# Kernel optimization log

Measured on AMD Instinct MI355X. Metric: run time of the kernel, lower is better.

## Reference

```python
import jax, jax.numpy as jnp
import numpy as np

D = 1024
H = 16
HD = D // H
L = 2048
B = 1
MLP = 8192
ROPE_BASE = 10000.0
LN_EPS = 1e-5


def layer_norm(x):
    mu = jnp.mean(x, axis=-1, keepdims=True)
    var = jnp.var(x, axis=-1, keepdims=True)
    return (x - mu) / jnp.sqrt(var + LN_EPS)


def rope(x):
    # x: [B, H, L, HD]; non-traditional (rotate-half / NeoX style)
    half = HD // 2
    inv_freq = 1.0 / (ROPE_BASE ** (jnp.arange(0, half, dtype=jnp.float32) / half))
    pos = jnp.arange(x.shape[2], dtype=jnp.float32)
    ang = pos[:, None] * inv_freq[None, :]            # [L, half]
    cos, sin = jnp.cos(ang), jnp.sin(ang)
    x1, x2 = x[..., :half], x[..., half:]
    return jnp.concatenate([x1 * cos - x2 * sin, x2 * cos + x1 * sin], axis=-1).astype(x.dtype)


def setup_inputs() -> dict:
    key = jax.random.key(0)
    ks = jax.random.split(key, 5)
    x = jax.random.normal(ks[0], (B, L, D), dtype=jnp.float32)
    # causal additive mask
    neg = jnp.finfo(jnp.float32).min
    mask = jnp.where(jnp.tril(jnp.ones((L, L), dtype=bool)), 0.0, neg).astype(jnp.float32)
    W_attn = jax.random.normal(ks[1], (3 * D, D), dtype=jnp.float32) * (D ** -0.5)
    W_out = jax.random.normal(ks[2], (D, D), dtype=jnp.float32) * (D ** -0.5)
    W_ffp = jax.random.normal(ks[3], (MLP, D), dtype=jnp.float32) * (D ** -0.5)
    W_ffo = jax.random.normal(ks[4], (D, MLP // 2), dtype=jnp.float32) * ((MLP // 2) ** -0.5)
    return {"x": x, "mask": mask, "W_attn": W_attn, "W_out": W_out, "W_ffp": W_ffp, "W_ffo": W_ffo}


def block(x, mask, W_attn, W_out, W_ffp, W_ffo):
    b, l, d = x.shape
    scale = HD ** -0.5
    # attention branch
    xn = layer_norm(x)
    qkv = xn @ W_attn.T                                    # [B, L, 3D]
    q, k, v = jnp.split(qkv, 3, axis=-1)
    q = q.reshape(b, l, H, HD).transpose(0, 2, 1, 3)       # [B, H, L, HD]
    k = k.reshape(b, l, H, HD).transpose(0, 2, 1, 3)
    v = v.reshape(b, l, H, HD).transpose(0, 2, 1, 3)
    q = rope(q)
    k = rope(k)
    scores = jnp.einsum('bhqd,bhkd->bhqk', q * scale, k)   # [B, H, L, L]
    scores = scores + mask
    probs = jax.nn.softmax(scores.astype(jnp.float32), axis=-1).astype(scores.dtype)
    attn = jnp.einsum('bhqk,bhkd->bhqd', probs, v)
    attn = attn.transpose(0, 2, 1, 3).reshape(b, l, d)
    r = attn @ W_out.T
    h = x + r
    # SwiGLU MLP branch: split ff_proj output, swiglu(x2, x1) = silu(x2) * x1
    g = layer_norm(h) @ W_ffp.T                            # [B, L, MLP]
    x1, x2 = jnp.split(g, 2, axis=-1)
    mlp = (jax.nn.silu(x2) * x1) @ W_ffo.T
    return h + mlp


def reference(x, mask, W_attn, W_out, W_ffp, W_ffo):
    return block(x, mask, W_attn, W_out, W_ffp, W_ffo)
```

## Files before the change

kernel.cpp:

```cpp
#include <hip/hip_runtime.h>
#include <math.h>

#define DMODEL 1024
#define NHEAD  16
#define HDIM   64
#define SEQ    2048
#define MLPD   8192
#define HALF_MLP 4096
static constexpr float LN_EPS_C = 1e-5f;
#define NEG_BIG (-1e30f)
#define SM_SHIFT 16.0f

typedef short bf16x8 __attribute__((ext_vector_type(8)));
typedef float f32x4  __attribute__((ext_vector_type(4)));

__device__ __forceinline__ unsigned short f2b(float f) {
    unsigned int u = __float_as_uint(f);
    u = (u + 0x7FFFu + ((u >> 16) & 1u)) >> 16;
    return (unsigned short)u;
}
__device__ __forceinline__ float b2f(unsigned short h) {
    return __uint_as_float((unsigned int)h << 16);
}

__device__ __forceinline__ void async_copy16(const unsigned short* g, unsigned short* l) {
    __builtin_amdgcn_global_load_lds(
        (const __attribute__((address_space(1))) unsigned int*)(g),
        (__attribute__((address_space(3))) unsigned int*)(l),
        16, 0, 0);
}

__global__ void prep_all(const float* __restrict__ x,
                         const float* __restrict__ W_attn, const float* __restrict__ W_out,
                         const float* __restrict__ W_ffp,  const float* __restrict__ W_ffo,
                         unsigned short* __restrict__ xnb, float2* __restrict__ ct,
                         unsigned short* __restrict__ oa, unsigned short* __restrict__ ob,
                         unsigned short* __restrict__ oc, unsigned short* __restrict__ od) {
    const int bid = blockIdx.x;
    const int tid = threadIdx.x;
    if (bid < SEQ) {
        __shared__ float rs[256], rs2[256];
        float4 v = *(const float4*)(x + (size_t)bid * DMODEL + tid * 4);
        rs[tid]  = v.x + v.y + v.z + v.w;
        rs2[tid] = v.x * v.x + v.y * v.y + v.z * v.z + v.w * v.w;
        __syncthreads();
        for (int off = 128; off > 0; off >>= 1) {
            if (tid < off) { rs[tid] += rs[tid + off]; rs2[tid] += rs2[tid + off]; }
            __syncthreads();
        }
        float mu  = rs[0] * (1.0f / DMODEL);
        float var = rs2[0] * (1.0f / DMODEL) - mu * mu;
        float inv = rsqrtf(var + LN_EPS_C);
        ushort4 o;
        o.x = f2b((v.x - mu) * inv); o.y = f2b((v.y - mu) * inv);
        o.z = f2b((v.z - mu) * inv); o.w = f2b((v.w - mu) * inv);
        *(ushort4*)(xnb + (size_t)bid * DMODEL + tid * 4) = o;
    } else if (bid < SEQ + 256) {
        int idx = (bid - SEQ) * 256 + tid;
        int pos = idx >> 5, p = idx & 31;
        float invf = powf(10000.0f, -(float)p / 32.0f);
        float ang = (float)pos * invf;
        ct[idx] = make_float2(cosf(ang), sinf(ang));
    } else {
        const int n1 = 3 * DMODEL * DMODEL;
        const int n2 = n1 + DMODEL * DMODEL;
        const int n3 = n2 + MLPD * DMODEL;
        int i = ((bid - SEQ - 256) * 256 + tid) * 4;
        const float* src; unsigned short* dst; int off;
        if (i < n1)      { src = W_attn; dst = oa; off = i; }
        else if (i < n2) { src = W_out;  dst = ob; off = i - n1; }
        else if (i < n3) {
            src = W_ffp; off = i - n2;
            int row = off >> 10, col = off & 1023;
            int rp  = (row < HALF_MLP) ? (2 * row) : (2 * (row - HALF_MLP) + 1);
            float4 v = *(const float4*)(src + off);
            ushort4 o;
            o.x = f2b(v.x); o.y = f2b(v.y); o.z = f2b(v.z); o.w = f2b(v.w);
            *(ushort4*)(oc + ((size_t)rp << 10) + col) = o;
            return;
        }
        else             { src = W_ffo; dst = od; off = i - n3; }
        float4 v = *(const float4*)(src + off);
        ushort4 o;
        o.x = f2b(v.x); o.y = f2b(v.y); o.z = f2b(v.z); o.w = f2b(v.w);
        *(ushort4*)(dst + off) = o;
    }
}

__global__ void ln_red2(const float* __restrict__ p0, const float* __restrict__ p1,
                        const float* __restrict__ x, float* __restrict__ h,
                        unsigned short* __restrict__ xnb) {
    const int row = blockIdx.x;
    const int tid = threadIdx.x;
    __shared__ float rs[256], rs2[256];
    const size_t base = (size_t)row * DMODEL + tid * 4;
    float4 a = *(const float4*)(p0 + base);
    float4 b = *(const float4*)(p1 + base);
    float4 r = *(const float4*)(x + base);
    float4 v = { a.x + b.x + r.x, a.y + b.y + r.y, a.z + b.z + r.z, a.w + b.w + r.w };
    *(float4*)(h + base) = v;
    rs[tid]  = v.x + v.y + v.z + v.w;
    rs2[tid] = v.x * v.x + v.y * v.y + v.z * v.z + v.w * v.w;
    __syncthreads();
    for (int off = 128; off > 0; off >>= 1) {
        if (tid < off) { rs[tid] += rs[tid + off]; rs2[tid] += rs2[tid + off]; }
        __syncthreads();
    }
    float mu  = rs[0] * (1.0f / DMODEL);
    float var = rs2[0] * (1.0f / DMODEL) - mu * mu;
    float inv = rsqrtf(var + LN_EPS_C);
    ushort4 o;
    o.x = f2b((v.x - mu) * inv); o.y = f2b((v.y - mu) * inv);
    o.z = f2b((v.z - mu) * inv); o.w = f2b((v.w - mu) * inv);
    *(ushort4*)(xnb + base) = o;
}

__global__ __launch_bounds__(256)
void gemm_qkv(const unsigned short* __restrict__ A, const unsigned short* __restrict__ B,
              const float2* __restrict__ ct,
              unsigned short* __restrict__ Qp, unsigned short* __restrict__ Kp,
              unsigned short* __restrict__ Vt) {
    __shared__ unsigned short As[128 * 32];
    __shared__ unsigned short Bs[128 * 32];
    __shared__ unsigned short St[4][16][72];
    const int tid  = threadIdx.x;
    const int lane = tid & 63;
    const int w    = tid >> 6;
    const int wm   = w >> 1;
    const int wn   = w & 1;
    const int m0   = blockIdx.y * 128;
    const int n0   = blockIdx.x * 128;

    f32x4 acc[4][4] = {};

    const int srow = lane >> 2;
    const int scol = (lane & 3) * 8;
    const unsigned short* Abase = A + (size_t)(m0 + w * 32 + srow) * DMODEL + scol;
    const unsigned short* Bbase = B + (size_t)(n0 + w * 32 + srow) * DMODEL + scol;
    unsigned short* AsW = &As[(w * 32) * 32];
    unsigned short* BsW = &Bs[(w * 32) * 32];

    const int fr = lane & 15;
    const int fk = (lane >> 4) * 8;

    for (int k0 = 0; k0 < DMODEL; k0 += 32) {
        async_copy16(Abase + k0,               AsW);
        async_copy16(Abase + k0 + 16 * DMODEL, AsW + 16 * 32);
        async_copy16(Bbase + k0,               BsW);
        async_copy16(Bbase + k0 + 16 * DMODEL, BsW + 16 * 32);
        __syncthreads();

        bf16x8 af[4], bfr[4];
#pragma unroll
        for (int i = 0; i < 4; ++i)
            af[i] = *(const bf16x8*)(&As[(wm * 64 + i * 16 + fr) * 32 + fk]);
#pragma unroll
        for (int j = 0; j < 4; ++j)
            bfr[j] = *(const bf16x8*)(&Bs[(wn * 64 + j * 16 + fr) * 32 + fk]);
#pragma unroll
        for (int i = 0; i < 4; ++i)
#pragma unroll
            for (int j = 0; j < 4; ++j)
                acc[i][j] = __builtin_amdgcn_mfma_f32_16x16x32_bf16(af[i], bfr[j], acc[i][j], 0, 0, 0);
        __syncthreads();
    }

    const int erow   = (lane >> 4) * 4;
    const int ecol   = lane & 15;
    const int region = blockIdx.x >> 3;
    const int head   = ((n0 + wn * 64) >> 6) & 15;

    if (region == 2) {
        const int sbase = m0 + wm * 64;
        const int dl = lane >> 3;
        const int ch = (lane & 7) * 8;
#pragma unroll
        for (int j = 0; j < 4; ++j) {
#pragma unroll
            for (int i = 0; i < 4; ++i) {
                ushort4 o;
                o.x = f2b(acc[i][j][0]); o.y = f2b(acc[i][j][1]);
                o.z = f2b(acc[i][j][2]); o.w = f2b(acc[i][j][3]);
                *(ushort4*)&St[w][ecol][i * 16 + erow] = o;
            }
#pragma unroll
            for (int p = 0; p < 2; ++p) {
                const int dd = p * 8 + dl;
                bf16x8 v = *(const bf16x8*)&St[w][dd][ch];
                *(bf16x8*)(Vt + ((size_t)head * HDIM + j * 16 + dd) * SEQ + sbase + ch) = v;
            }
        }
    } else {
        unsigned short* P = region ? Kp : Qp;
        const float scale = region ? 1.0f : 0.125f;
        unsigned short* qb = &St[w][erow][0];
#pragma unroll
        for (int i = 0; i < 4; ++i) {
#pragma unroll
            for (int r = 0; r < 4; ++r) {
                const int rowg = m0 + wm * 64 + i * 16 + erow + r;
                const float2* crow = ct + (size_t)rowg * 32;
#pragma unroll
                for (int jj = 0; jj < 2; ++jj) {
                    const float2 cs = crow[jj * 16 + ecol];
                    const float x1 = acc[i][jj][r];
                    const float x2 = acc[i][jj + 2][r];
                    qb[jj * 16 + ecol]      = f2b((x1 * cs.x - x2 * cs.y) * scale);
                    qb[jj * 16 + ecol + 32] = f2b((x2 * cs.x + x1 * cs.y) * scale);
                }
                ushort4 o = *(const ushort4*)&qb[ecol * 4];
                *(ushort4*)(P + ((size_t)head * SEQ + rowg) * HDIM + ecol * 4) = o;
            }
        }
    }
}

__global__ __launch_bounds__(256)
void gemm_mfma_sk(const unsigned short* __restrict__ A, const unsigned short* __restrict__ B,
                  float* __restrict__ P, int Ksub, int lda, int ldb, int ldc) {
    __shared__ unsigned short As[128 * 32];
    __shared__ unsigned short Bs[128 * 32];
    const int tid  = threadIdx.x;
    const int lane = tid & 63;
    const int w    = tid >> 6;
    const int wm   = w >> 1;
    const int wn   = w & 1;
    const int m0   = blockIdx.y * 128;
    const int n0   = blockIdx.x * 128;
    const int kb   = blockIdx.z * Ksub;

    f32x4 acc[4][4] = {};

    const int srow = lane >> 2;
    const int scol = (lane & 3) * 8;
    const unsigned short* Abase = A + (size_t)(m0 + w * 32 + srow) * lda + scol + kb;
    const unsigned short* Bbase = B + (size_t)(n0 + w * 32 + srow) * ldb + scol + kb;
    unsigned short* AsW = &As[(w * 32) * 32];
    unsigned short* BsW = &Bs[(w * 32) * 32];

    const int fr = lane & 15;
    const int fk = (lane >> 4) * 8;

    for (int k0 = 0; k0 < Ksub; k0 += 32) {
        async_copy16(Abase + k0,            AsW);
        async_copy16(Abase + k0 + 16 * lda, AsW + 16 * 32);
        async_copy16(Bbase + k0,            BsW);
        async_copy16(Bbase + k0 + 16 * (size_t)ldb, BsW + 16 * 32);
        __syncthreads();

        bf16x8 af[4], bfr[4];
#pragma unroll
        for (int i = 0; i < 4; ++i)
            af[i] = *(const bf16x8*)(&As[(wm * 64 + i * 16 + fr) * 32 + fk]);
#pragma unroll
        for (int j = 0; j < 4; ++j)
            bfr[j] = *(const bf16x8*)(&Bs[(wn * 64 + j * 16 + fr) * 32 + fk]);
#pragma unroll
        for (int i = 0; i < 4; ++i)
#pragma unroll
            for (int j = 0; j < 4; ++j)
                acc[i][j] = __builtin_amdgcn_mfma_f32_16x16x32_bf16(af[i], bfr[j], acc[i][j], 0, 0, 0);
        __syncthreads();
    }

    float* Pp = P + (size_t)blockIdx.z * SEQ * ldc;
    const int erow = (lane >> 4) * 4;
    const int ecol = lane & 15;
#pragma unroll
    for (int i = 0; i < 4; ++i)
#pragma unroll
        for (int j = 0; j < 4; ++j) {
            const int colg = n0 + wn * 64 + j * 16 + ecol;
#pragma unroll
            for (int r = 0; r < 4; ++r) {
                const int rowg = m0 + wm * 64 + i * 16 + erow + r;
                Pp[(size_t)rowg * ldc + colg] = acc[i][j][r];
            }
        }
}

__global__ void reduce4_kernel(const float* __restrict__ p0, const float* __restrict__ p1,
                               const float* __restrict__ p2, const float* __restrict__ p3,
                               const float* __restrict__ res, float* __restrict__ out) {
    int i = (blockIdx.x * blockDim.x + threadIdx.x) * 4;
    float4 a = *(const float4*)(p0 + i);
    float4 b = *(const float4*)(p1 + i);
    float4 c = *(const float4*)(p2 + i);
    float4 d = *(const float4*)(p3 + i);
    float4 r = *(const float4*)(res + i);
    float4 o = { a.x + b.x + c.x + d.x + r.x, a.y + b.y + c.y + d.y + r.y,
                 a.z + b.z + c.z + d.z + r.z, a.w + b.w + c.w + d.w + r.w };
    *(float4*)(out + i) = o;
}

#define STW 40
__global__ __launch_bounds__(256)
void gemm_ffp_silu(const unsigned short* __restrict__ A, const unsigned short* __restrict__ B,
                   unsigned short* __restrict__ gact) {
    __shared__ unsigned short As[128 * 32];
    __shared__ unsigned short Bs[128 * 32];
    __shared__ unsigned short St[4][64][STW];
    const int tid  = threadIdx.x;
    const int lane = tid & 63;
    const int w    = tid >> 6;
    const int wm   = w >> 1;
    const int wn   = w & 1;
    const int m0   = blockIdx.y * 128;
    const int n0   = blockIdx.x * 128;

    f32x4 acc[4][4] = {};

    const int srow = lane >> 2;
    const int scol = (lane & 3) * 8;
    const unsigned short* Abase = A + (size_t)(m0 + w * 32 + srow) * DMODEL + scol;
    const unsigned short* Bbase = B + (size_t)(n0 + w * 32 + srow) * DMODEL + scol;
    unsigned short* AsW = &As[(w * 32) * 32];
    unsigned short* BsW = &Bs[(w * 32) * 32];

    const int fr = lane & 15;
    const int fk = (lane >> 4) * 8;

    for (int k0 = 0; k0 < DMODEL; k0 += 32) {
        async_copy16(Abase + k0,               AsW);
        async_copy16(Abase + k0 + 16 * DMODEL, AsW + 16 * 32);
        async_copy16(Bbase + k0,               BsW);
        async_copy16(Bbase + k0 + 16 * DMODEL, BsW + 16 * 32);
        __syncthreads();

        bf16x8 af[4], bfr[4];
#pragma unroll
        for (int i = 0; i < 4; ++i)
            af[i] = *(const bf16x8*)(&As[(wm * 64 + i * 16 + fr) * 32 + fk]);
#pragma unroll
        for (int j = 0; j < 4; ++j)
            bfr[j] = *(const bf16x8*)(&Bs[(wn * 64 + j * 16 + fr) * 32 + fk]);
#pragma unroll
        for (int i = 0; i < 4; ++i)
#pragma unroll
            for (int j = 0; j < 4; ++j)
                acc[i][j] = __builtin_amdgcn_mfma_f32_16x16x32_bf16(af[i], bfr[j], acc[i][j], 0, 0, 0);
        __syncthreads();
    }

    const int erow = (lane >> 4) * 4;
    const int ecol = lane & 15;
    const bool evn = (ecol & 1) == 0;
#pragma unroll
    for (int i = 0; i < 4; ++i)
#pragma unroll
        for (int j = 0; j < 4; ++j)
#pragma unroll
            for (int r = 0; r < 4; ++r) {
                float own = acc[i][j][r];
                float oth = __shfl_xor(own, 1);
                if (evn) {
                    float sil = oth / (1.0f + __expf(-oth));
                    St[w][i * 16 + erow + r][j * 8 + (ecol >> 1)] = f2b(sil * own);
                }
            }
    {
        const int rowg = m0 + wm * 64 + lane;
        unsigned short* dst = gact + (size_t)rowg * HALF_MLP + (n0 >> 1) + wn * 32;
        bf16x8 v0 = *(const bf16x8*)&St[w][lane][0];
        bf16x8 v1 = *(const bf16x8*)&St[w][lane][8];
        bf16x8 v2 = *(const bf16x8*)&St[w][lane][16];
        bf16x8 v3 = *(const bf16x8*)&St[w][lane][24];
        *(bf16x8*)(dst + 0)  = v0;
        *(bf16x8*)(dst + 8)  = v1;
        *(bf16x8*)(dst + 16) = v2;
        *(bf16x8*)(dst + 24) = v3;
    }
}

__global__ __launch_bounds__(256)
void fattn_wave(const unsigned short* __restrict__ Qp,
                const unsigned short* __restrict__ Kp,
                const unsigned short* __restrict__ Vt,
                unsigned short* __restrict__ out) {
    __shared__ unsigned short Ps[4][16][72];
    const int head = blockIdx.y;
    const int tid  = threadIdx.x;
    const int lane = tid & 63;
    const int w    = tid >> 6;
    const int fr   = lane & 15;
    const int quad = lane >> 4;

    const int u  = blockIdx.x * 4 + w;
    const int mt = (u & 1) ? (127 - (u >> 1)) : (u >> 1);
    const int m0 = mt * 16;

    const unsigned short* Qg = Qp + (size_t)head * SEQ * HDIM;
    const unsigned short* Kg = Kp + (size_t)head * SEQ * HDIM;
    const unsigned short* Vg = Vt + (size_t)head * HDIM * SEQ;

    bf16x8 qf[2];
#pragma unroll
    for (int kk = 0; kk < 2; ++kk)
        qf[kk] = *(const bf16x8*)(Qg + (size_t)(m0 + fr) * HDIM + kk * 32 + quad * 8);

    bf16x8 ones;
#pragma unroll
    for (int e = 0; e < 8; ++e) ones[e] = (short)0x3F80;

    f32x4 accO[4] = {};
    f32x4 accL = {};

    const int nkeys = m0 + 16;
    for (int j0 = 0; j0 < nkeys; j0 += 64) {
        f32x4 accS[4] = {};
#pragma unroll
        for (int kk = 0; kk < 2; ++kk) {
#pragma unroll
            for (int j = 0; j < 4; ++j) {
                bf16x8 kf = *(const bf16x8*)(Kg + (size_t)(j0 + j * 16 + fr) * HDIM + kk * 32 + quad * 8);
                accS[j] = __builtin_amdgcn_mfma_f32_16x16x32_bf16(qf[kk], kf, accS[j], 0, 0, 0);
            }
        }

        if (j0 + 64 >= nkeys) {
#pragma unroll
            for (int j = 0; j < 4; ++j)
#pragma unroll
                for (int r = 0; r < 4; ++r)
                    if (j0 + j * 16 + fr > m0 + quad * 4 + r) accS[j][r] = NEG_BIG;
        }

#pragma unroll
        for (int j = 0; j < 4; ++j)
#pragma unroll
            for (int r = 0; r < 4; ++r)
                Ps[w][quad * 4 + r][j * 16 + fr] = f2b(__expf(accS[j][r] - SM_SHIFT));

#pragma unroll
        for (int kk = 0; kk < 2; ++kk) {
            bf16x8 pf = *(const bf16x8*)&Ps[w][fr][kk * 32 + quad * 8];
            accL = __builtin_amdgcn_mfma_f32_16x16x32_bf16(pf, ones, accL, 0, 0, 0);
#pragma unroll
            for (int j = 0; j < 4; ++j) {
                bf16x8 vf = *(const bf16x8*)(Vg + (size_t)(j * 16 + fr) * SEQ + j0 + kk * 32 + quad * 8);
                accO[j] = __builtin_amdgcn_mfma_f32_16x16x32_bf16(pf, vf, accO[j], 0, 0, 0);
            }
        }
    }

#pragma unroll
    for (int r = 0; r < 4; ++r) {
        const float inv = 1.0f / accL[r];
        const int qrow = m0 + quad * 4 + r;
#pragma unroll
        for (int j = 0; j < 4; ++j)
            out[(size_t)qrow * DMODEL + head * HDIM + j * 16 + fr] = f2b(accO[j][r] * inv);
    }
}

extern "C" void kernel_launch(void* const* d_in, const int* in_sizes, int n_in,
                              void* d_out, int out_size, void* d_ws, size_t ws_size,
                              hipStream_t stream) {
    const float* x      = (const float*)d_in[0];
    const float* W_attn = (const float*)d_in[2];
    const float* W_out  = (const float*)d_in[3];
    const float* W_ffp  = (const float*)d_in[4];
    const float* W_ffo  = (const float*)d_in[5];
    float* out = (float*)d_out;

    char* wsb = (char*)d_ws;
    unsigned short* wb_attn = (unsigned short*)(wsb);
    unsigned short* wb_out  = (unsigned short*)(wsb + (6u  << 20));
    unsigned short* wb_ffp  = (unsigned short*)(wsb + (8u  << 20));
    unsigned short* wb_ffo  = (unsigned short*)(wsb + (24u << 20));
    float*          h       = (float*)(wsb + (32u << 20));
    unsigned short* xnb     = (unsigned short*)(wsb + (40u << 20));
    unsigned short* attnb   = (unsigned short*)(wsb + (44u << 20));
    unsigned short* gact    = (unsigned short*)(wsb + (48u << 20));
    unsigned short* Qp      = (unsigned short*)(wsb + (64u << 20));
    unsigned short* Kp      = (unsigned short*)(wsb + (68u << 20));
    unsigned short* Vt      = (unsigned short*)(wsb + (72u << 20));
    float*          wout_p  = (float*)(wsb + (76u << 20));
    float2*         ct      = (float2*)(wsb + (92u << 20));
    float*          ffo_p   = (float*)(wsb + (64u << 20));

    {
        int f2b_blocks = (3 * DMODEL * DMODEL + DMODEL * DMODEL + MLPD * DMODEL
                          + DMODEL * HALF_MLP) / 4 / 256;
        prep_all<<<SEQ + 256 + f2b_blocks, 256, 0, stream>>>(
            x, W_attn, W_out, W_ffp, W_ffo, xnb, ct,
            wb_attn, wb_out, wb_ffp, wb_ffo);
    }

    gemm_qkv<<<dim3(3 * DMODEL / 128, SEQ / 128), 256, 0, stream>>>(
        xnb, wb_attn, ct, Qp, Kp, Vt);

    fattn_wave<<<dim3(SEQ / 64, NHEAD), 256, 0, stream>>>(Qp, Kp, Vt, attnb);

    gemm_mfma_sk<<<dim3(DMODEL / 128, SEQ / 128, 2), 256, 0, stream>>>(
        attnb, wb_out, wout_p, DMODEL / 2, DMODEL, DMODEL, DMODEL);

    ln_red2<<<SEQ, 256, 0, stream>>>(wout_p, wout_p + (size_t)SEQ * DMODEL, x, h, xnb);

    gemm_ffp_silu<<<dim3(MLPD / 128, SEQ / 128), 256, 0, stream>>>(
        xnb, wb_ffp, gact);

    gemm_mfma_sk<<<dim3(DMODEL / 128, SEQ / 128, 4), 256, 0, stream>>>(
        gact, wb_ffo, ffo_p, HALF_MLP / 4, HALF_MLP, HALF_MLP, DMODEL);

    reduce4_kernel<<<SEQ * DMODEL / 4 / 256, 256, 0, stream>>>(
        ffo_p, ffo_p + (size_t)SEQ * DMODEL, ffo_p + 2 * (size_t)SEQ * DMODEL,
        ffo_p + 3 * (size_t)SEQ * DMODEL, h, out);
}
```

Baseline: 338.8 us.

## Split attention over key tiles into four partial passes plus combine kernel

```diff
diff --git a/kernel.cpp b/kernel.cpp
--- a/kernel.cpp
+++ b/kernel.cpp
@@ -10,6 +10,7 @@
 static constexpr float LN_EPS_C = 1e-5f;
 #define NEG_BIG (-1e30f)
 #define SM_SHIFT 16.0f
+#define NSPLIT 4
 
 typedef short bf16x8 __attribute__((ext_vector_type(8)));
 typedef float f32x4  __attribute__((ext_vector_type(4)));
@@ -373,12 +374,14 @@
 }
 
 __global__ __launch_bounds__(256)
-void fattn_wave(const unsigned short* __restrict__ Qp,
-                const unsigned short* __restrict__ Kp,
-                const unsigned short* __restrict__ Vt,
-                unsigned short* __restrict__ out) {
+void fattn_wave_sk(const unsigned short* __restrict__ Qp,
+                   const unsigned short* __restrict__ Kp,
+                   const unsigned short* __restrict__ Vt,
+                   float* __restrict__ PO01, float* __restrict__ PO23,
+                   float* __restrict__ PL) {
     __shared__ unsigned short Ps[4][16][72];
     const int head = blockIdx.y;
+    const int s    = blockIdx.z;
     const int tid  = threadIdx.x;
     const int lane = tid & 63;
     const int w    = tid >> 6;
@@ -405,8 +408,10 @@
     f32x4 accO[4] = {};
     f32x4 accL = {};
 
-    const int nkeys = m0 + 16;
-    for (int j0 = 0; j0 < nkeys; j0 += 64) {
+    const int nkeys  = m0 + 16;
+    const int ntiles = (nkeys + 63) >> 6;
+    for (int t = s; t < ntiles; t += NSPLIT) {
+        const int j0 = t * 64;
         f32x4 accS[4] = {};
 #pragma unroll
         for (int kk = 0; kk < 2; ++kk) {
@@ -417,7 +422,7 @@
             }
         }
 
-        if (j0 + 64 >= nkeys) {
+        if (t == ntiles - 1) {
 #pragma unroll
             for (int j = 0; j < 4; ++j)
 #pragma unroll
@@ -443,14 +448,43 @@
         }
     }
 
+    const size_t OSTRIDE = (size_t)NHEAD * SEQ * HDIM;
+    float* POh = (s < 2 ? PO01 + (size_t)s * OSTRIDE
+                        : PO23 + (size_t)(s - 2) * OSTRIDE)
+                 + (size_t)head * SEQ * HDIM;
+    float* PLh = PL + ((size_t)s * NHEAD + head) * SEQ;
 #pragma unroll
     for (int r = 0; r < 4; ++r) {
-        const float inv = 1.0f / accL[r];
         const int qrow = m0 + quad * 4 + r;
+        if (fr == 0) PLh[qrow] = accL[r];
 #pragma unroll
         for (int j = 0; j < 4; ++j)
-            out[(size_t)qrow * DMODEL + head * HDIM + j * 16 + fr] = f2b(accO[j][r] * inv);
-    }
+            POh[(size_t)qrow * HDIM + j * 16 + fr] = accO[j][r];
+    }
+}
+
+__global__ void attn_combine(const float* __restrict__ PO01, const float* __restrict__ PO23,
+                             const float* __restrict__ PL, unsigned short* __restrict__ out) {
+    const int qrow = blockIdx.x;
+    const int tid  = threadIdx.x;
+    const int head = tid >> 4;
+    const int c0   = (tid & 15) * 4;
+    const size_t ostride = (size_t)NHEAD * SEQ * HDIM;
+    const size_t base = ((size_t)head * SEQ + qrow) * HDIM + c0;
+    float4 a = *(const float4*)(PO01 + base);
+    float4 b = *(const float4*)(PO01 + ostride + base);
+    float4 c = *(const float4*)(PO23 + base);
+    float4 d = *(const float4*)(PO23 + ostride + base);
+    const size_t lb = (size_t)head * SEQ + qrow;
+    float l = PL[lb] + PL[(size_t)NHEAD * SEQ + lb]
+            + PL[2 * (size_t)NHEAD * SEQ + lb] + PL[3 * (size_t)NHEAD * SEQ + lb];
+    float inv = 1.0f / l;
+    ushort4 o;
+    o.x = f2b((a.x + b.x + c.x + d.x) * inv);
+    o.y = f2b((a.y + b.y + c.y + d.y) * inv);
+    o.z = f2b((a.z + b.z + c.z + d.z) * inv);
+    o.w = f2b((a.w + b.w + c.w + d.w) * inv);
+    *(ushort4*)(out + (size_t)qrow * DMODEL + head * HDIM + c0) = o;
 }
 
 extern "C" void kernel_launch(void* const* d_in, const int* in_sizes, int n_in,
@@ -479,6 +513,10 @@
     float2*         ct      = (float2*)(wsb + (92u << 20));
     float*          ffo_p   = (float*)(wsb + (64u << 20));
 
+    float* attn_po01 = (float*)gact;
+    float* attn_po23 = wout_p;
+    float* attn_pl   = h;
+
     {
         int f2b_blocks = (3 * DMODEL * DMODEL + DMODEL * DMODEL + MLPD * DMODEL
                           + DMODEL * HALF_MLP) / 4 / 256;
@@ -490,7 +528,10 @@
     gemm_qkv<<<dim3(3 * DMODEL / 128, SEQ / 128), 256, 0, stream>>>(
         xnb, wb_attn, ct, Qp, Kp, Vt);
 
-    fattn_wave<<<dim3(SEQ / 64, NHEAD), 256, 0, stream>>>(Qp, Kp, Vt, attnb);
+    fattn_wave_sk<<<dim3(SEQ / 64, NHEAD, NSPLIT), 256, 0, stream>>>(
+        Qp, Kp, Vt, attn_po01, attn_po23, attn_pl);
+
+    attn_combine<<<SEQ, 256, 0, stream>>>(attn_po01, attn_po23, attn_pl, attnb);
 
     gemm_mfma_sk<<<dim3(DMODEL / 128, SEQ / 128, 2), 256, 0, stream>>>(
         attnb, wb_out, wout_p, DMODEL / 2, DMODEL, DMODEL, DMODEL);
```

Measured after the change: 360.8 us. 6.5% more time.

## Share K/V tiles across waves via double-buffered LDS in flash attention

Applied to the files above, without the earlier changes.

```diff
diff --git a/kernel.cpp b/kernel.cpp
--- a/kernel.cpp
+++ b/kernel.cpp
@@ -373,26 +373,32 @@
 }
 
 __global__ __launch_bounds__(256)
-void fattn_wave(const unsigned short* __restrict__ Qp,
-                const unsigned short* __restrict__ Kp,
-                const unsigned short* __restrict__ Vt,
-                unsigned short* __restrict__ out) {
+void fattn_blk(const unsigned short* __restrict__ Qp,
+               const unsigned short* __restrict__ Kp,
+               const unsigned short* __restrict__ Vt,
+               unsigned short* __restrict__ out) {
+    __shared__ unsigned short Ks[2][64][64];
+    __shared__ unsigned short Vs[2][64][64];
     __shared__ unsigned short Ps[4][16][72];
-    const int head = blockIdx.y;
     const int tid  = threadIdx.x;
     const int lane = tid & 63;
     const int w    = tid >> 6;
     const int fr   = lane & 15;
     const int quad = lane >> 4;
 
-    const int u  = blockIdx.x * 4 + w;
-    const int mt = (u & 1) ? (127 - (u >> 1)) : (u >> 1);
-    const int m0 = mt * 16;
+    const int f    = blockIdx.x;
+    const int head = ((f & 7) << 1) | ((f >> 3) & 1);
+    const int ub   = f >> 4;
+    const int qb   = (ub & 1) ? (31 - (ub >> 1)) : (ub >> 1);
+    const int m0   = qb * 64 + w * 16;
 
     const unsigned short* Qg = Qp + (size_t)head * SEQ * HDIM;
     const unsigned short* Kg = Kp + (size_t)head * SEQ * HDIM;
     const unsigned short* Vg = Vt + (size_t)head * HDIM * SEQ;
 
+    const int rA = (w << 3) + (lane >> 3);
+    const int cg = ((lane & 7) ^ ((lane >> 3) & 7)) << 3;
+
     bf16x8 qf[2];
 #pragma unroll
     for (int kk = 0; kk < 2; ++kk)
@@ -405,19 +411,47 @@
     f32x4 accO[4] = {};
     f32x4 accL = {};
 
-    const int nkeys = m0 + 16;
-    for (int j0 = 0; j0 < nkeys; j0 += 64) {
+    const int ntiles = qb + 1;
+
+    {
+        const unsigned short* gk = Kg + (size_t)rA * HDIM + cg;
+        unsigned short* dk = &Ks[0][w << 3][0];
+        async_copy16(gk, dk);
+        async_copy16(gk + 32 * HDIM, dk + 32 * 64);
+        const unsigned short* gv = Vg + (size_t)rA * SEQ + cg;
+        unsigned short* dv = &Vs[0][w << 3][0];
+        async_copy16(gv, dv);
+        async_copy16(gv + 32 * SEQ, dv + 32 * 64);
+    }
+    __syncthreads();
+
+    int cur = 0;
+    for (int t = 0; t < ntiles; ++t) {
+        if (t + 1 < ntiles) {
+            const int j1 = (t + 1) * 64;
+            const unsigned short* gk = Kg + (size_t)(j1 + rA) * HDIM + cg;
+            unsigned short* dk = &Ks[cur ^ 1][w << 3][0];
+            async_copy16(gk, dk);
+            async_copy16(gk + 32 * HDIM, dk + 32 * 64);
+            const unsigned short* gv = Vg + (size_t)rA * SEQ + j1 + cg;
+            unsigned short* dv = &Vs[cur ^ 1][w << 3][0];
+            async_copy16(gv, dv);
+            async_copy16(gv + 32 * SEQ, dv + 32 * 64);
+        }
+
+        const int j0 = t * 64;
         f32x4 accS[4] = {};
 #pragma unroll
         for (int kk = 0; kk < 2; ++kk) {
 #pragma unroll
             for (int j = 0; j < 4; ++j) {
-                bf16x8 kf = *(const bf16x8*)(Kg + (size_t)(j0 + j * 16 + fr) * HDIM + kk * 32 + quad * 8);
+                bf16x8 kf = *(const bf16x8*)
+                    &Ks[cur][j * 16 + fr][(((kk << 2) + quad) ^ (fr & 7)) << 3];
                 accS[j] = __builtin_amdgcn_mfma_f32_16x16x32_bf16(qf[kk], kf, accS[j], 0, 0, 0);
             }
         }
 
-        if (j0 + 64 >= nkeys) {
+        if (t == ntiles - 1) {
 #pragma unroll
             for (int j = 0; j < 4; ++j)
 #pragma unroll
@@ -437,10 +471,14 @@
             accL = __builtin_amdgcn_mfma_f32_16x16x32_bf16(pf, ones, accL, 0, 0, 0);
 #pragma unroll
             for (int j = 0; j < 4; ++j) {
-                bf16x8 vf = *(const bf16x8*)(Vg + (size_t)(j * 16 + fr) * SEQ + j0 + kk * 32 + quad * 8);
+                bf16x8 vf = *(const bf16x8*)
+                    &Vs[cur][j * 16 + fr][(((kk << 2) + quad) ^ (fr & 7)) << 3];
                 accO[j] = __builtin_amdgcn_mfma_f32_16x16x32_bf16(pf, vf, accO[j], 0, 0, 0);
             }
         }
+
+        __syncthreads();
+        cur ^= 1;
     }
 
 #pragma unroll
@@ -490,7 +528,7 @@
     gemm_qkv<<<dim3(3 * DMODEL / 128, SEQ / 128), 256, 0, stream>>>(
         xnb, wb_attn, ct, Qp, Kp, Vt);
 
-    fattn_wave<<<dim3(SEQ / 64, NHEAD), 256, 0, stream>>>(Qp, Kp, Vt, attnb);
+    fattn_blk<<<512, 256, 0, stream>>>(Qp, Kp, Vt, attnb);
 
     gemm_mfma_sk<<<dim3(DMODEL / 128, SEQ / 128, 2), 256, 0, stream>>>(
         attnb, wb_out, wout_p, DMODEL / 2, DMODEL, DMODEL, DMODEL);
```

Result: faster. 310.9 us (-8.2%).
